# Performance work log

Measured on AMD Instinct MI355X. Metric: run time of the kernel, lower is better.

The kernel has to match this reference:

```python
import jax, jax.numpy as jnp
import numpy as np

B, S, D, H = 4, 2048, 1024, 16
HD = D // H
ROPE_THETA = 10000.0


def setup_inputs() -> dict:
    key = jax.random.key(0)
    ks = jax.random.split(key, 5)
    scale = 1.0 / np.sqrt(D)
    inp = {
        "x": jax.random.normal(ks[0], (B, S, D), dtype=jnp.float32),
        "Wq": jax.random.normal(ks[1], (D, D), dtype=jnp.float32) * scale,
        "bq": jnp.zeros((D,), jnp.float32),
        "Wk": jax.random.normal(ks[2], (D, D), dtype=jnp.float32) * scale,
        "bk": jnp.zeros((D,), jnp.float32),
        "Wv": jax.random.normal(ks[3], (D, D), dtype=jnp.float32) * scale,
        "bv": jnp.zeros((D,), jnp.float32),
        "Wo": jax.random.normal(ks[4], (D, D), dtype=jnp.float32) * scale,
        "bo": jnp.zeros((D,), jnp.float32),
        # causal mask: True means masked (j > i), matching masked_fill semantics
        "attn_mask": jnp.triu(jnp.ones((S, S), dtype=bool), k=1),
    }
    return inp


def _rope(x):
    # x: [B, H, S, HD]; half-split rotary embedding
    half = HD // 2
    inv_freq = 1.0 / (ROPE_THETA ** (jnp.arange(0, half, dtype=jnp.float32) / half))
    pos = jnp.arange(x.shape[2], dtype=jnp.float32)
    freqs = pos[:, None] * inv_freq[None, :]            # [S, half]
    cos = jnp.cos(freqs)[None, None]                    # [1,1,S,half]
    sin = jnp.sin(freqs)[None, None]
    x1, x2 = x[..., :half], x[..., half:]
    return jnp.concatenate([x1 * cos - x2 * sin, x2 * cos + x1 * sin], axis=-1)


def reference(x, Wq, bq, Wk, bk, Wv, bv, Wo, bo, attn_mask):
    def shape(t):  # [B,S,D] -> [B,H,S,HD]
        return t.reshape(B, S, H, HD).transpose(0, 2, 1, 3)

    q = shape(x @ Wq.T + bq)
    k = shape(x @ Wk.T + bk)
    v = shape(x @ Wv.T + bv)
    q = _rope(q)
    k = _rope(k)
    scores = jnp.einsum("bhqd,bhkd->bhqk", q, k) * (HD ** -0.5)
    scores = jnp.where(attn_mask[None, None], -jnp.inf, scores)
    w = jax.nn.softmax(scores, axis=-1)
    attn = jnp.einsum("bhqk,bhkd->bhqd", w, v)
    merged = attn.transpose(0, 2, 1, 3).reshape(B, S, D)
    return merged @ Wo.T + bo
```

## Files before the change

kernel.cpp:

```cpp
#include <hip/hip_runtime.h>
#include <math.h>

#define BATCH 4
#define SEQ   2048
#define DMODEL 1024
#define NHEAD 16
#define HDIM  64
#define MROWS (BATCH*SEQ)

typedef unsigned short u16;
typedef unsigned int   u32;

using bf16x8 = __attribute__((ext_vector_type(8))) short;
using f32x4  = __attribute__((ext_vector_type(4))) float;
using f32x16 = __attribute__((ext_vector_type(16))) float;
using u32x4  = __attribute__((ext_vector_type(4))) unsigned int;

__device__ __forceinline__ u16 f2bf(float f) {
    u32 u = __float_as_uint(f);
    u += 0x7fffu + ((u >> 16) & 1u);
    return (u16)(u >> 16);
}
__device__ __forceinline__ u32 pack2bf(float a, float b) {
    u32 ua = __float_as_uint(a); ua += 0x7fffu + ((ua >> 16) & 1u);
    u32 ub = __float_as_uint(b); ub += 0x7fffu + ((ub >> 16) & 1u);
    return (ua >> 16) | (ub & 0xffff0000u);
}
__device__ __forceinline__ u32 cvtpk(float a, float b) {
    u32 r;
    asm("v_cvt_pk_bf16_f32 %0, %1, %2" : "=v"(r) : "v"(a), "v"(b));
    return r;
}
#define PLSWAP(a, b) asm("v_permlane32_swap_b32 %0, %1" : "+v"(a), "+v"(b))

#define GLOBAL_LOAD_LDS16(gp, lp)                                              \
    __builtin_amdgcn_global_load_lds(                                          \
        (const __attribute__((address_space(1))) void*)(gp),                   \
        (__attribute__((address_space(3))) void*)(lp), 16, 0, 0)

__global__ __launch_bounds__(256) void convert_inputs(
    const float* __restrict__ x,  const float* __restrict__ wq,
    const float* __restrict__ wk, const float* __restrict__ wv,
    const float* __restrict__ wo, u16* __restrict__ dst)
{
    long long i4 = ((long long)blockIdx.x * 256 + threadIdx.x) * 4;
    const float* src; long long off;
    if (i4 < 8388608LL) { src = x; off = i4; }
    else {
        long long j = i4 - 8388608LL;
        int seg = (int)(j >> 20);
        off = j & 1048575LL;
        src = (seg == 0) ? wq : (seg == 1) ? wk : (seg == 2) ? wv : wo;
    }
    float4 v = *(const float4*)(src + off);
    u32 lo = (u32)f2bf(v.x) | ((u32)f2bf(v.y) << 16);
    u32 hi = (u32)f2bf(v.z) | ((u32)f2bf(v.w) << 16);
    *(uint2*)(dst + i4) = make_uint2(lo, hi);
}

template<int QKV>
__global__ __launch_bounds__(512) void gemm_mfma(
    const u16* __restrict__ A,
    const u16* __restrict__ Wq_, const u16* __restrict__ Wk_, const u16* __restrict__ Wv_,
    const float* __restrict__ bq_, const float* __restrict__ bk_, const float* __restrict__ bv_,
    u16* __restrict__ Cq_, u16* __restrict__ Ck_, u16* __restrict__ Cv_,
    float* __restrict__ Cf)
{
    __shared__ __align__(16) u16 smem[65536];

    const int t    = threadIdx.x;
    const int lane = t & 63;
    const int w    = t >> 6;
    const int quad = lane >> 4;
    const int l15  = lane & 15;
    const int wm   = w >> 2;
    const int wn   = w & 3;

    const int bx  = blockIdx.x;
    const int xcd = bx & 7;
    const int i_  = bx >> 3;
    const int bml = i_ & 3;
    const int n_  = i_ >> 2;
    const int seg = (QKV ? (n_ >> 2) : 0);
    const int nn  = (QKV ? (n_ & 3) : n_);

    const u16*   W    = (seg == 0) ? Wq_ : (seg == 1) ? Wk_ : Wv_;
    const float* bias = (seg == 0) ? bq_ : (seg == 1) ? bk_ : bv_;
    u16*         Cb   = (seg == 0) ? Cq_ : (seg == 1) ? Ck_ : Cv_;

    const int bm = (xcd * 4 + bml) * 256;
    const int bn = nn * 256;

    const int sr8 = lane >> 3;
    const int scl = (lane & 7) ^ sr8;
    const u16* gA = A + (size_t)(bm + 8 * w + sr8) * DMODEL + scl * 8;
    const u16* gB = W + (size_t)(bn + 8 * w + sr8) * DMODEL + scl * 8;

#define STG_A(rg, kt, bs)                                                      \
    GLOBAL_LOAD_LDS16(gA + (size_t)(rg) * 64 * DMODEL + (kt) * 64,             \
                      &smem[(bs) * 16384 + ((rg) * 64 + 8 * w) * 64])
#define STG_B(rg, kt, bs)                                                      \
    GLOBAL_LOAD_LDS16(gB + (size_t)(rg) * 64 * DMODEL + (kt) * 64,             \
                      &smem[32768 + (bs) * 16384 + ((rg) * 64 + 8 * w) * 64])

    STG_B(0, 0, 0); STG_B(1, 0, 0); STG_B(2, 0, 0); STG_B(3, 0, 0);
    STG_A(0, 0, 0); STG_A(2, 0, 0); STG_A(1, 0, 0); STG_A(3, 0, 0);
    STG_B(0, 1, 1); STG_B(1, 1, 1); STG_B(2, 1, 1); STG_B(3, 1, 1);
    STG_A(0, 1, 1); STG_A(2, 1, 1);
    asm volatile("s_waitcnt vmcnt(6)" ::: "memory");
    __builtin_amdgcn_s_barrier();

    const int cA0 = (quad ^ (l15 & 7)) * 8;

    f32x4 acc[8][4] = {};
    bf16x8 bfr[4][2];

#define LOAD_B(Bb) {                                                           \
    _Pragma("unroll")                                                          \
    for (int j = 0; j < 4; ++j) {                                              \
        bfr[j][0] = *(const bf16x8*)&(Bb)[(wn * 64 + 16 * j + l15) * 64 + cA0];\
        bfr[j][1] = *(const bf16x8*)&(Bb)[(wn * 64 + 16 * j + l15) * 64 + (cA0 ^ 32)];\
    } }
#define PHASE(q, Ab, Bb, STAGES, CKPT) {                                       \
    bf16x8 af_[2][2];                                                          \
    if ((q) == 0) LOAD_B(Bb);                                                  \
    _Pragma("unroll")                                                          \
    for (int ii = 0; ii < 2; ++ii) {                                           \
        const int r_ = (wm * 128 + (q) * 32 + 16 * ii + l15) * 64;             \
        af_[ii][0] = *(const bf16x8*)&(Ab)[r_ + cA0];                          \
        af_[ii][1] = *(const bf16x8*)&(Ab)[r_ + (cA0 ^ 32)];                   \
    }                                                                          \
    STAGES;                                                                    \
    __builtin_amdgcn_s_barrier();                                              \
    asm volatile("s_waitcnt lgkmcnt(0)" ::: "memory");                         \
    __builtin_amdgcn_sched_barrier(0);                                         \
    __builtin_amdgcn_s_setprio(1);                                             \
    _Pragma("unroll")                                                          \
    for (int ii = 0; ii < 2; ++ii)                                             \
        _Pragma("unroll")                                                      \
        for (int j = 0; j < 4; ++j) {                                          \
            acc[2*(q)+ii][j] = __builtin_amdgcn_mfma_f32_16x16x32_bf16(        \
                af_[ii][0], bfr[j][0], acc[2*(q)+ii][j], 0, 0, 0);             \
            acc[2*(q)+ii][j] = __builtin_amdgcn_mfma_f32_16x16x32_bf16(        \
                af_[ii][1], bfr[j][1], acc[2*(q)+ii][j], 0, 0, 0);             \
        }                                                                      \
    __builtin_amdgcn_s_setprio(0);                                             \
    CKPT;                                                                      \
    __builtin_amdgcn_s_barrier();                                              \
}

    #pragma unroll 1
    for (int i = 0; i < 8; ++i) {
        const bool st = (i < 7);
        const int  kn = 2 * i + 2, kn3 = 2 * i + 3, ko = 2 * i + 1;
        {
            const u16* Ab = smem;
            const u16* Bb = smem + 32768;
            PHASE(0, Ab, Bb, { STG_A(1, ko, 1); STG_A(3, ko, 1); }, {});
            PHASE(1, Ab, Bb, { if (st) { STG_B(0, kn, 0); STG_B(1, kn, 0); } }, {});
            PHASE(2, Ab, Bb, { if (st) { STG_B(2, kn, 0); STG_B(3, kn, 0); } }, {});
            PHASE(3, Ab, Bb, { if (st) { STG_A(0, kn, 0); STG_A(2, kn, 0); } },
                  { if (st) asm volatile("s_waitcnt vmcnt(6)" ::: "memory");
                    else    asm volatile("s_waitcnt vmcnt(0)" ::: "memory"); });
        }
        {
            const u16* Ab = smem + 16384;
            const u16* Bb = smem + 32768 + 16384;
            PHASE(0, Ab, Bb, { if (st) { STG_A(1, kn, 0); STG_A(3, kn, 0); } }, {});
            PHASE(1, Ab, Bb, { if (st) { STG_B(0, kn3, 1); STG_B(1, kn3, 1); } }, {});
            PHASE(2, Ab, Bb, { if (st) { STG_B(2, kn3, 1); STG_B(3, kn3, 1); } }, {});
            PHASE(3, Ab, Bb, { if (st) { STG_A(0, kn3, 1); STG_A(2, kn3, 1); } },
                  { if (st) asm volatile("s_waitcnt vmcnt(6)" ::: "memory");
                    else    asm volatile("s_waitcnt vmcnt(0)" ::: "memory"); });
        }
    }
#undef PHASE
#undef LOAD_B
#undef STG_A
#undef STG_B

    const int wrow = wm * 128;
    const int wcol = wn * 64;
    float bvv[4];
    #pragma unroll
    for (int j = 0; j < 4; j++) bvv[j] = bias[bn + wcol + 16 * j + l15];

    if constexpr (QKV == 0) {
        #pragma unroll
        for (int ri = 0; ri < 8; ri++)
            #pragma unroll
            for (int r = 0; r < 4; r++) {
                int mg = bm + wrow + 16 * ri + quad * 4 + r;
                #pragma unroll
                for (int j = 0; j < 4; j++)
                    Cf[(size_t)mg * DMODEL + bn + wcol + 16 * j + l15] = acc[ri][j][r] + bvv[j];
            }
    } else {
        if (seg == 2) {
            u16* T = smem;
            #pragma unroll
            for (int ri = 0; ri < 8; ri++) {
                #pragma unroll
                for (int j = 0; j < 4; j++) {
                    int col = wrow + 16 * ri + quad * 4;
                    int row = wcol + 16 * j + l15;
                    u32 lo = pack2bf(acc[ri][j][0] + bvv[j], acc[ri][j][1] + bvv[j]);
                    u32 hi = pack2bf(acc[ri][j][2] + bvv[j], acc[ri][j][3] + bvv[j]);
                    *(uint2*)((char*)T + row * 512 + ((col * 2) ^ ((row & 7) << 4)))
                        = make_uint2(lo, hi);
                }
            }
            __syncthreads();
            {
                int row = t >> 1, half = t & 1;
                int hgl = (bn + row) >> 6;
                int dl  = (bn + row) & 63;
                int bb  = bm >> 11;
                size_t obase = (((size_t)(bb * NHEAD + hgl)) * HDIM + dl) * SEQ
                             + (bm & (SEQ - 1)) + half * 128;
                #pragma unroll
                for (int k = 0; k < 16; k++) {
                    uint4 vv = *(const uint4*)((const char*)T + row * 512
                                 + ((half * 256 + k * 16) ^ ((row & 7) << 4)));
                    *(uint4*)(Cb + obase + k * 8) = vv;
                }
            }
        } else {
            const float qscale = (seg == 0) ? 0.18033688011112042f : 1.0f;
            float inv[2];
            #pragma unroll
            for (int j = 0; j < 2; j++) {
                int d = 16 * j + l15;
                inv[j] = exp2f(-(float)d * 0.4152410118609203f);
            }
            #pragma unroll
            for (int ri = 0; ri < 8; ri++)
                #pragma unroll
                for (int r = 0; r < 4; r++) {
                    int mg = bm + wrow + 16 * ri + quad * 4 + r;
                    int s  = mg & (SEQ - 1);
                    #pragma unroll
                    for (int j = 0; j < 2; j++) {
                        float f = (float)s * inv[j];
                        float sn, cs;
                        __sincosf(f, &sn, &cs);
                        float a1 = acc[ri][j][r]     + bvv[j];
                        float a2 = acc[ri][j + 2][r] + bvv[j + 2];
                        float o1 = (a1 * cs - a2 * sn) * qscale;
                        float o2 = (a2 * cs + a1 * sn) * qscale;
                        Cb[(size_t)mg * DMODEL + bn + wcol + 16 * j       + l15] = f2bf(o1);
                        Cb[(size_t)mg * DMODEL + bn + wcol + 16 * (j + 2) + l15] = f2bf(o2);
                    }
                }
        }
    }
}

__global__ __launch_bounds__(256) void attn_mfma(
    const u16* __restrict__ Q, const u16* __restrict__ K,
    const u16* __restrict__ VT, u16* __restrict__ O)
{
    __shared__ __align__(16) u16 smem[16640];
    u16* const Qs  = smem;
    u16* const Ks0 = smem + 8192;
    u16* const Ks1 = smem;
    u16* const Vt0 = smem + 12288;
    u16* const Vt1 = smem + 4096;
    float* const lS = (float*)(smem + 16384);

    const int t    = threadIdx.x;
    const int lane = t & 63;
    const int w    = t >> 6;
    const int l31  = lane & 31;
    const int hl   = lane >> 5;
    const int bid  = blockIdx.x;
    const int bh   = bid & 63;
    const int x_   = bid >> 6, g_ = x_ >> 2, r_ = x_ & 3;
    const int qt   = (g_ == 0) ? 15 - r_ : (g_ == 1) ? 8 + r_
                   : (g_ == 2) ? 4 + r_ : 3 - r_;
    const int h    = bh & (NHEAD - 1);
    const int b    = bh >> 4;
    const int q0   = qt * 128;

    const size_t gbase = ((size_t)b * SEQ) * DMODEL + h * HDIM;
    const size_t vbase = ((size_t)(b * NHEAD + h)) * HDIM * SEQ;

    const int rl  = lane >> 3;
    const int csw = (lane & 7) ^ rl;

    #pragma unroll
    for (int i = 0; i < 4; i++) {
        int row = 32 * w + 8 * i + rl;
        GLOBAL_LOAD_LDS16(Q + gbase + (size_t)(q0 + row) * DMODEL + csw * 8,
                          &Qs[(32 * w + 8 * i) * 64]);
    }
    #pragma unroll
    for (int i = 0; i < 2; i++) {
        int row = 16 * w + 8 * i + rl;
        GLOBAL_LOAD_LDS16(K + gbase + (size_t)row * DMODEL + csw * 8,
                          &Ks0[(16 * w + 8 * i) * 64]);
        GLOBAL_LOAD_LDS16(VT + vbase + (size_t)row * SEQ + csw * 8,
                          &Vt0[(16 * w + 8 * i) * 64]);
    }
    __syncthreads();

    bf16x8 qf[4];
    {
        int row = 32 * w + l31;
        #pragma unroll
        for (int s = 0; s < 4; s++) {
            int c = (hl + 2 * s) ^ (row & 7);
            qf[s] = *(const bf16x8*)&Qs[row * 64 + c * 8];
        }
    }
    __syncthreads();

    float lsum = 0.0f;
    f32x16 oacc[2] = {};
    const int qg   = q0 + 32 * w + l31;
    const int qmax = q0 + 32 * w + 31;

#define QUADRANT(KRH, F0, F1) do {                                             \
    f32x16 s_ = {};                                                            \
    __builtin_amdgcn_s_setprio(1);                                             \
    _Pragma("unroll")                                                          \
    for (int stp_ = 0; stp_ < 4; ++stp_) {                                     \
        int c_ = ((hl + 2 * stp_) ^ (l31 & 7)) * 8;                            \
        bf16x8 ka_ = *(const bf16x8*)&Ksb[(32 * (KRH) + l31) * 64 + c_];       \
        s_ = __builtin_amdgcn_mfma_f32_32x32x16_bf16(ka_, qf[stp_], s_, 0, 0, 0);\
    }                                                                          \
    __builtin_amdgcn_s_setprio(0);                                             \
    if (k0 + 32 * (KRH) + 31 > q0 + 32 * w) {                                  \
        _Pragma("unroll")                                                      \
        for (int rr_ = 0; rr_ < 16; ++rr_) {                                   \
            int krg_ = k0 + 32 * (KRH) + (rr_ & 3) + 8 * (rr_ >> 2) + 4 * hl;  \
            if (krg_ > qg) s_[rr_] = -1e30f;                                   \
        }                                                                      \
    }                                                                          \
    float pv_[16];                                                             \
    _Pragma("unroll")                                                          \
    for (int rr_ = 0; rr_ < 16; ++rr_) pv_[rr_] = __builtin_amdgcn_exp2f(s_[rr_]);\
    lsum += ((pv_[0]+pv_[1])+(pv_[2]+pv_[3])) + ((pv_[4]+pv_[5])+(pv_[6]+pv_[7]))\
          + ((pv_[8]+pv_[9])+(pv_[10]+pv_[11])) + ((pv_[12]+pv_[13])+(pv_[14]+pv_[15]));\
    u32 k01_ = cvtpk(pv_[0], pv_[1]),   k23_ = cvtpk(pv_[2], pv_[3]);          \
    u32 k45_ = cvtpk(pv_[4], pv_[5]),   k67_ = cvtpk(pv_[6], pv_[7]);          \
    u32 k89_ = cvtpk(pv_[8], pv_[9]),   kab_ = cvtpk(pv_[10], pv_[11]);        \
    u32 kcd_ = cvtpk(pv_[12], pv_[13]), kef_ = cvtpk(pv_[14], pv_[15]);        \
    PLSWAP(k01_, k45_); PLSWAP(k23_, k67_);                                    \
    PLSWAP(k89_, kcd_); PLSWAP(kab_, kef_);                                    \
    { union { u32x4 u; bf16x8 v; } c0_; c0_.u = (u32x4){k01_, k23_, k45_, k67_};\
      F0 = c0_.v; }                                                            \
    { union { u32x4 u; bf16x8 v; } c1_; c1_.u = (u32x4){k89_, kab_, kcd_, kef_};\
      F1 = c1_.v; }                                                            \
} while (0)

#define PVSTEP(STP, PF) do {                                                   \
    int c_ = ((hl + 2 * (STP)) ^ (l31 & 7)) * 8;                               \
    bf16x8 v0_ = *(const bf16x8*)&Vtb[l31 * 64 + c_];                          \
    bf16x8 v1_ = *(const bf16x8*)&Vtb[(32 + l31) * 64 + c_];                   \
    oacc[0] = __builtin_amdgcn_mfma_f32_32x32x16_bf16(PF, v0_, oacc[0], 0, 0, 0);\
    oacc[1] = __builtin_amdgcn_mfma_f32_32x32x16_bf16(PF, v1_, oacc[1], 0, 0, 0);\
} while (0)

    const int ktn = 2 * qt + 2;
    for (int kt = 0; kt < ktn; kt++) {
        const int k0 = kt * 64;
        u16* const Ksb = (kt & 1) ? Ks1 : Ks0;
        u16* const Vtb = (kt & 1) ? Vt1 : Vt0;

        if (kt + 1 < ktn) {
            u16* const Ksn = (kt & 1) ? Ks0 : Ks1;
            u16* const Vtn = (kt & 1) ? Vt0 : Vt1;
            const size_t kk0 = (size_t)(kt + 1) * 64;
            #pragma unroll
            for (int i = 0; i < 2; i++) {
                int row = 16 * w + 8 * i + rl;
                GLOBAL_LOAD_LDS16(K + gbase + (kk0 + row) * DMODEL + csw * 8,
                                  &Ksn[(16 * w + 8 * i) * 64]);
                GLOBAL_LOAD_LDS16(VT + vbase + (size_t)row * SEQ + kk0 + csw * 8,
                                  &Vtn[(16 * w + 8 * i) * 64]);
            }
        }

        if (k0 <= qmax) {
            const bool q2 = (k0 + 32 <= qmax);
            bf16x8 pa0, pa1, pa2, pa3;
            QUADRANT(0, pa0, pa1);
            __builtin_amdgcn_s_setprio(1);
            PVSTEP(0, pa0); PVSTEP(1, pa1);
            __builtin_amdgcn_s_setprio(0);
            if (q2) {
                QUADRANT(1, pa2, pa3);
                __builtin_amdgcn_s_setprio(1);
                PVSTEP(2, pa2); PVSTEP(3, pa3);
                __builtin_amdgcn_s_setprio(0);
            }
        }
        asm volatile("s_waitcnt vmcnt(0)" ::: "memory");
        __builtin_amdgcn_s_barrier();
    }
#undef QUADRANT
#undef PVSTEP

    lsum += __shfl_xor(lsum, 32, 64);
    if (lane < 32) lS[32 * w + lane] = lsum;
    __syncthreads();

    #pragma unroll
    for (int g = 0; g < 4; g++) {
        f32x4 lv = *(const f32x4*)&lS[32 * w + 8 * g + 4 * hl];
        #pragma unroll
        for (int rr = 0; rr < 4; rr++) {
            int qg2 = q0 + 32 * w + rr + 8 * g + 4 * hl;
            float inv = 1.0f / lv[rr];
            #pragma unroll
            for (int dh = 0; dh < 2; dh++) {
                float o = oacc[dh][4 * g + rr] * inv;
                O[gbase + (size_t)qg2 * DMODEL + 32 * dh + l31] = f2bf(o);
            }
        }
    }
}

extern "C" void kernel_launch(void* const* d_in, const int* in_sizes, int n_in,
                              void* d_out, int out_size, void* d_ws, size_t ws_size,
                              hipStream_t stream)
{
    const float* x  = (const float*)d_in[0];
    const float* Wq = (const float*)d_in[1];
    const float* bq = (const float*)d_in[2];
    const float* Wk = (const float*)d_in[3];
    const float* bk = (const float*)d_in[4];
    const float* Wv = (const float*)d_in[5];
    const float* bv = (const float*)d_in[6];
    const float* Wo = (const float*)d_in[7];
    const float* bo = (const float*)d_in[8];

    u16* wsp = (u16*)d_ws;
    u16* xb  = wsp;
    u16* Wqb = wsp + 8388608;
    u16* Wkb = Wqb + 1048576;
    u16* Wvb = Wkb + 1048576;
    u16* Wob = Wvb + 1048576;
    u16* Qb  = Wob + 1048576;
    u16* Kb  = Qb + 8388608;
    u16* Vb  = Kb + 8388608;
    u16* Ab  = Vb + 8388608;

    convert_inputs<<<12288, 256, 0, stream>>>(x, Wq, Wk, Wv, Wo, xb);

    gemm_mfma<1><<<384, 512, 0, stream>>>(xb, Wqb, Wkb, Wvb, bq, bk, bv,
                                          Qb, Kb, Vb, nullptr);

    attn_mfma<<<1024, 256, 0, stream>>>(Qb, Kb, Vb, Ab);

    gemm_mfma<0><<<128, 512, 0, stream>>>(Ab, Wob, nullptr, nullptr, bo, nullptr, nullptr,
                                          nullptr, nullptr, nullptr, (float*)d_out);
}
```

Baseline: 265.4 us.

## Split QKV GEMM and use 256x128 tiles for V and output projections

Replaces the single 384-block QKV GEMM with a 256-block Q/K GEMM (Wq and Wk addressed as one contiguous 2048-row weight) plus a separate V GEMM. The V GEMM and the output projection now use a new kernel with 256x128 tiles and a three-stage LDS ring buffer, which gives the output projection 256 blocks instead of 128. The intent is better CU occupancy on a GPU with many CUs and fewer wave-quantization tails. The cost is an extra kernel launch and lower arithmetic intensity per tile in the narrower GEMM.

```diff
diff --git a/kernel.cpp b/kernel.cpp
--- a/kernel.cpp
+++ b/kernel.cpp
@@ -58,13 +58,10 @@
     *(uint2*)(dst + i4) = make_uint2(lo, hi);
 }
 
-template<int QKV>
-__global__ __launch_bounds__(512) void gemm_mfma(
-    const u16* __restrict__ A,
-    const u16* __restrict__ Wq_, const u16* __restrict__ Wk_, const u16* __restrict__ Wv_,
-    const float* __restrict__ bq_, const float* __restrict__ bk_, const float* __restrict__ bv_,
-    u16* __restrict__ Cq_, u16* __restrict__ Ck_, u16* __restrict__ Cv_,
-    float* __restrict__ Cf)
+__global__ __launch_bounds__(512) void gemm_qk(
+    const u16* __restrict__ A, const u16* __restrict__ Wqk,
+    const float* __restrict__ bq_, const float* __restrict__ bk_,
+    u16* __restrict__ Cq_, u16* __restrict__ Ck_)
 {
     __shared__ __align__(16) u16 smem[65536];
 
@@ -81,20 +78,19 @@
     const int i_  = bx >> 3;
     const int bml = i_ & 3;
     const int n_  = i_ >> 2;
-    const int seg = (QKV ? (n_ >> 2) : 0);
-    const int nn  = (QKV ? (n_ & 3) : n_);
-
-    const u16*   W    = (seg == 0) ? Wq_ : (seg == 1) ? Wk_ : Wv_;
-    const float* bias = (seg == 0) ? bq_ : (seg == 1) ? bk_ : bv_;
-    u16*         Cb   = (seg == 0) ? Cq_ : (seg == 1) ? Ck_ : Cv_;
 
     const int bm = (xcd * 4 + bml) * 256;
-    const int bn = nn * 256;
+    const int bn = n_ * 256;
+
+    const bool  isq  = (bn < 1024);
+    const float* bias = isq ? bq_ : bk_;
+    u16*         Cb   = isq ? Cq_ : Ck_;
+    const int    bnl  = bn & 1023;
 
     const int sr8 = lane >> 3;
     const int scl = (lane & 7) ^ sr8;
-    const u16* gA = A + (size_t)(bm + 8 * w + sr8) * DMODEL + scl * 8;
-    const u16* gB = W + (size_t)(bn + 8 * w + sr8) * DMODEL + scl * 8;
+    const u16* gA = A   + (size_t)(bm + 8 * w + sr8) * DMODEL + scl * 8;
+    const u16* gB = Wqk + (size_t)(bn + 8 * w + sr8) * DMODEL + scl * 8;
 
 #define STG_A(rg, kt, bs)                                                      \
     GLOBAL_LOAD_LDS16(gA + (size_t)(rg) * 64 * DMODEL + (kt) * 64,             \
@@ -183,75 +179,197 @@
     const int wcol = wn * 64;
     float bvv[4];
     #pragma unroll
-    for (int j = 0; j < 4; j++) bvv[j] = bias[bn + wcol + 16 * j + l15];
-
-    if constexpr (QKV == 0) {
+    for (int j = 0; j < 4; j++) bvv[j] = bias[bnl + wcol + 16 * j + l15];
+
+    const float qscale = isq ? 0.18033688011112042f : 1.0f;
+    float inv[2];
+    #pragma unroll
+    for (int j = 0; j < 2; j++) {
+        int d = 16 * j + l15;
+        inv[j] = exp2f(-(float)d * 0.4152410118609203f);
+    }
+    #pragma unroll
+    for (int ri = 0; ri < 8; ri++)
+        #pragma unroll
+        for (int r = 0; r < 4; r++) {
+            int mg = bm + wrow + 16 * ri + quad * 4 + r;
+            int s  = mg & (SEQ - 1);
+            #pragma unroll
+            for (int j = 0; j < 2; j++) {
+                float f = (float)s * inv[j];
+                float sn, cs;
+                __sincosf(f, &sn, &cs);
+                float a1 = acc[ri][j][r]     + bvv[j];
+                float a2 = acc[ri][j + 2][r] + bvv[j + 2];
+                float o1 = (a1 * cs - a2 * sn) * qscale;
+                float o2 = (a2 * cs + a1 * sn) * qscale;
+                Cb[(size_t)mg * DMODEL + bnl + wcol + 16 * j       + l15] = f2bf(o1);
+                Cb[(size_t)mg * DMODEL + bnl + wcol + 16 * (j + 2) + l15] = f2bf(o2);
+            }
+        }
+}
+
+template<int EPI>
+__global__ __launch_bounds__(512) void gemm_nj2(
+    const u16* __restrict__ A, const u16* __restrict__ W,
+    const float* __restrict__ bias_, u16* __restrict__ Cb, float* __restrict__ Cf)
+{
+    __shared__ __align__(16) u16 smem[73728];
+
+    const int t    = threadIdx.x;
+    const int lane = t & 63;
+    const int w    = t >> 6;
+    const int quad = lane >> 4;
+    const int l15  = lane & 15;
+    const int wm   = w >> 2;
+    const int wn   = w & 3;
+
+    const int bx  = blockIdx.x;
+    const int xcd = bx & 7;
+    const int i_  = bx >> 3;
+    const int bml = i_ & 3;
+    const int n_  = i_ >> 2;
+
+    const int bm = (xcd * 4 + bml) * 256;
+    const int bn = n_ * 128;
+
+    const int sr8 = lane >> 3;
+    const int scl = (lane & 7) ^ sr8;
+    const u16* gA = A + (size_t)(bm + 8 * w + sr8) * DMODEL + scl * 8;
+    const u16* gB = W + (size_t)(bn + 8 * w + sr8) * DMODEL + scl * 8;
+
+#define STG_A(rg, kt, bs)                                                      \
+    GLOBAL_LOAD_LDS16(gA + (size_t)(rg) * 64 * DMODEL + (kt) * 64,             \
+                      &smem[(bs) * 16384 + ((rg) * 64 + 8 * w) * 64])
+#define STG_B(rg, kt, bs)                                                      \
+    GLOBAL_LOAD_LDS16(gB + (size_t)(rg) * 64 * DMODEL + (kt) * 64,             \
+                      &smem[49152 + (bs) * 8192 + ((rg) * 64 + 8 * w) * 64])
+
+    STG_B(0, 0, 0); STG_B(1, 0, 0);
+    STG_A(0, 0, 0); STG_A(1, 0, 0); STG_A(2, 0, 0); STG_A(3, 0, 0);
+    STG_B(0, 1, 1); STG_B(1, 1, 1);
+    STG_A(0, 1, 1); STG_A(1, 1, 1); STG_A(2, 1, 1); STG_A(3, 1, 1);
+    asm volatile("s_waitcnt vmcnt(6)" ::: "memory");
+    __builtin_amdgcn_s_barrier();
+
+    const int cA0 = (quad ^ (l15 & 7)) * 8;
+
+    f32x4 acc[8][2] = {};
+
+    int c = 0;
+    #pragma unroll 1
+    for (int kt = 0; kt < 16; ++kt) {
+        const u16* Ab = smem + c * 16384;
+        const u16* Bb = smem + 49152 + c * 8192;
+        const int  sb = (c >= 1) ? c - 1 : 2;
+        const int  ks = kt + 2;
+        const bool st = (kt < 14);
+
+        bf16x8 bfr[2][2], af[4][2];
+
+        #pragma unroll
+        for (int j = 0; j < 2; ++j) {
+            bfr[j][0] = *(const bf16x8*)&Bb[(wn * 32 + 16 * j + l15) * 64 + cA0];
+            bfr[j][1] = *(const bf16x8*)&Bb[(wn * 32 + 16 * j + l15) * 64 + (cA0 ^ 32)];
+        }
+        #pragma unroll
+        for (int ii = 0; ii < 4; ++ii) {
+            const int r_ = (wm * 128 + 16 * ii + l15) * 64;
+            af[ii][0] = *(const bf16x8*)&Ab[r_ + cA0];
+            af[ii][1] = *(const bf16x8*)&Ab[r_ + (cA0 ^ 32)];
+        }
+        if (st) { STG_B(0, ks, sb); STG_B(1, ks, sb); STG_A(0, ks, sb); }
+        __builtin_amdgcn_s_barrier();
+        asm volatile("s_waitcnt lgkmcnt(0)" ::: "memory");
+        __builtin_amdgcn_sched_barrier(0);
+        __builtin_amdgcn_s_setprio(1);
+        #pragma unroll
+        for (int ii = 0; ii < 4; ++ii)
+            #pragma unroll
+            for (int j = 0; j < 2; ++j) {
+                acc[ii][j] = __builtin_amdgcn_mfma_f32_16x16x32_bf16(
+                    af[ii][0], bfr[j][0], acc[ii][j], 0, 0, 0);
+                acc[ii][j] = __builtin_amdgcn_mfma_f32_16x16x32_bf16(
+                    af[ii][1], bfr[j][1], acc[ii][j], 0, 0, 0);
+            }
+        __builtin_amdgcn_s_setprio(0);
+        __builtin_amdgcn_s_barrier();
+
+        #pragma unroll
+        for (int ii = 0; ii < 4; ++ii) {
+            const int r_ = (wm * 128 + 64 + 16 * ii + l15) * 64;
+            af[ii][0] = *(const bf16x8*)&Ab[r_ + cA0];
+            af[ii][1] = *(const bf16x8*)&Ab[r_ + (cA0 ^ 32)];
+        }
+        if (st) { STG_A(1, ks, sb); STG_A(2, ks, sb); STG_A(3, ks, sb); }
+        __builtin_amdgcn_s_barrier();
+        asm volatile("s_waitcnt lgkmcnt(0)" ::: "memory");
+        __builtin_amdgcn_sched_barrier(0);
+        __builtin_amdgcn_s_setprio(1);
+        #pragma unroll
+        for (int ii = 0; ii < 4; ++ii)
+            #pragma unroll
+            for (int j = 0; j < 2; ++j) {
+                acc[4 + ii][j] = __builtin_amdgcn_mfma_f32_16x16x32_bf16(
+                    af[ii][0], bfr[j][0], acc[4 + ii][j], 0, 0, 0);
+                acc[4 + ii][j] = __builtin_amdgcn_mfma_f32_16x16x32_bf16(
+                    af[ii][1], bfr[j][1], acc[4 + ii][j], 0, 0, 0);
+            }
+        __builtin_amdgcn_s_setprio(0);
+        if (st) asm volatile("s_waitcnt vmcnt(6)" ::: "memory");
+        else    asm volatile("s_waitcnt vmcnt(0)" ::: "memory");
+        __builtin_amdgcn_s_barrier();
+
+        c = (c == 2) ? 0 : c + 1;
+    }
+#undef STG_A
+#undef STG_B
+
+    const int wrow = wm * 128;
+    const int wcol = wn * 32;
+    float bvv[2];
+    #pragma unroll
+    for (int j = 0; j < 2; j++) bvv[j] = bias_[bn + wcol + 16 * j + l15];
+
+    if constexpr (EPI == 0) {
         #pragma unroll
         for (int ri = 0; ri < 8; ri++)
             #pragma unroll
             for (int r = 0; r < 4; r++) {
                 int mg = bm + wrow + 16 * ri + quad * 4 + r;
                 #pragma unroll
-                for (int j = 0; j < 4; j++)
+                for (int j = 0; j < 2; j++)
                     Cf[(size_t)mg * DMODEL + bn + wcol + 16 * j + l15] = acc[ri][j][r] + bvv[j];
             }
     } else {
-        if (seg == 2) {
-            u16* T = smem;
-            #pragma unroll
-            for (int ri = 0; ri < 8; ri++) {
-                #pragma unroll
-                for (int j = 0; j < 4; j++) {
-                    int col = wrow + 16 * ri + quad * 4;
-                    int row = wcol + 16 * j + l15;
-                    u32 lo = pack2bf(acc[ri][j][0] + bvv[j], acc[ri][j][1] + bvv[j]);
-                    u32 hi = pack2bf(acc[ri][j][2] + bvv[j], acc[ri][j][3] + bvv[j]);
-                    *(uint2*)((char*)T + row * 512 + ((col * 2) ^ ((row & 7) << 4)))
-                        = make_uint2(lo, hi);
-                }
-            }
-            __syncthreads();
-            {
-                int row = t >> 1, half = t & 1;
-                int hgl = (bn + row) >> 6;
-                int dl  = (bn + row) & 63;
-                int bb  = bm >> 11;
-                size_t obase = (((size_t)(bb * NHEAD + hgl)) * HDIM + dl) * SEQ
-                             + (bm & (SEQ - 1)) + half * 128;
-                #pragma unroll
-                for (int k = 0; k < 16; k++) {
-                    uint4 vv = *(const uint4*)((const char*)T + row * 512
-                                 + ((half * 256 + k * 16) ^ ((row & 7) << 4)));
-                    *(uint4*)(Cb + obase + k * 8) = vv;
-                }
-            }
-        } else {
-            const float qscale = (seg == 0) ? 0.18033688011112042f : 1.0f;
-            float inv[2];
+        u16* T = smem;
+        __syncthreads();
+        #pragma unroll
+        for (int ri = 0; ri < 8; ri++) {
             #pragma unroll
             for (int j = 0; j < 2; j++) {
-                int d = 16 * j + l15;
-                inv[j] = exp2f(-(float)d * 0.4152410118609203f);
-            }
-            #pragma unroll
-            for (int ri = 0; ri < 8; ri++)
-                #pragma unroll
-                for (int r = 0; r < 4; r++) {
-                    int mg = bm + wrow + 16 * ri + quad * 4 + r;
-                    int s  = mg & (SEQ - 1);
-                    #pragma unroll
-                    for (int j = 0; j < 2; j++) {
-                        float f = (float)s * inv[j];
-                        float sn, cs;
-                        __sincosf(f, &sn, &cs);
-                        float a1 = acc[ri][j][r]     + bvv[j];
-                        float a2 = acc[ri][j + 2][r] + bvv[j + 2];
-                        float o1 = (a1 * cs - a2 * sn) * qscale;
-                        float o2 = (a2 * cs + a1 * sn) * qscale;
-                        Cb[(size_t)mg * DMODEL + bn + wcol + 16 * j       + l15] = f2bf(o1);
-                        Cb[(size_t)mg * DMODEL + bn + wcol + 16 * (j + 2) + l15] = f2bf(o2);
-                    }
-                }
+                int col = wrow + 16 * ri + quad * 4;
+                int row = wcol + 16 * j + l15;
+                u32 lo = pack2bf(acc[ri][j][0] + bvv[j], acc[ri][j][1] + bvv[j]);
+                u32 hi = pack2bf(acc[ri][j][2] + bvv[j], acc[ri][j][3] + bvv[j]);
+                *(uint2*)((char*)T + row * 512 + ((col * 2) ^ ((row & 7) << 4)))
+                    = make_uint2(lo, hi);
+            }
+        }
+        __syncthreads();
+        {
+            int row = t >> 2, colc = t & 3;
+            int hgl = (bn + row) >> 6;
+            int dl  = (bn + row) & 63;
+            int bb  = bm >> 11;
+            size_t obase = (((size_t)(bb * NHEAD + hgl)) * HDIM + dl) * SEQ
+                         + (bm & (SEQ - 1)) + colc * 64;
+            #pragma unroll
+            for (int k = 0; k < 8; k++) {
+                uint4 vv = *(const uint4*)((const char*)T + row * 512
+                             + ((colc * 128 + k * 16) ^ ((row & 7) << 4)));
+                *(uint4*)(Cb + obase + k * 8) = vv;
+            }
         }
     }
 }
@@ -449,11 +567,11 @@
 
     convert_inputs<<<12288, 256, 0, stream>>>(x, Wq, Wk, Wv, Wo, xb);
 
-    gemm_mfma<1><<<384, 512, 0, stream>>>(xb, Wqb, Wkb, Wvb, bq, bk, bv,
-                                          Qb, Kb, Vb, nullptr);
+    gemm_qk<<<256, 512, 0, stream>>>(xb, Wqb, bq, bk, Qb, Kb);
+
+    gemm_nj2<1><<<256, 512, 0, stream>>>(xb, Wvb, bv, Vb, nullptr);
 
     attn_mfma<<<1024, 256, 0, stream>>>(Qb, Kb, Vb, Ab);
 
-    gemm_mfma<0><<<128, 512, 0, stream>>>(Ab, Wob, nullptr, nullptr, bo, nullptr, nullptr,
-                                          nullptr, nullptr, nullptr, (float*)d_out);
-}
+    gemm_nj2<0><<<256, 512, 0, stream>>>(Ab, Wob, bo, nullptr, (float*)d_out);
+}
```

Result: faster. 254.3 us (-4.2%).
